# Optimization experiments

Hardware: AMD Instinct MI355X
Metric: run time of the kernel (lower is better)

## Reference

```python
import jax, jax.numpy as jnp
import numpy as np

B, S, H = 2, 1024, 1024
NH, NKV, HD = 16, 4, 64
E, TOPK, I = 8, 2, 3584
EPS = 1e-5
THETA = 1e6


def setup_inputs() -> dict:
    key = jax.random.key(0)
    ks = jax.random.split(key, 12)
    def w(k, shape, fan_in):
        return jax.random.normal(k, shape, dtype=jnp.float32) * (1.0 / np.sqrt(fan_in))
    return {
        "hidden_states": jax.random.normal(ks[0], (B, S, H), dtype=jnp.float32),
        "position_ids": jnp.broadcast_to(jnp.arange(S, dtype=jnp.int64)[None, :], (B, S)),
        "ln1_w": jnp.ones((H,), jnp.float32),
        "ln2_w": jnp.ones((H,), jnp.float32),
        "wq": w(ks[1], (H, NH * HD), H),
        "wk": w(ks[2], (H, NKV * HD), H),
        "wv": w(ks[3], (H, NKV * HD), H),
        "wo": w(ks[4], (NH * HD, H), NH * HD),
        "router_w": w(ks[5], (H, E), H),
        "w_gate": w(ks[6], (E, H, I), H),
        "w_up": w(ks[7], (E, H, I), H),
        "w_down": w(ks[8], (E, I, H), I),
    }


def _rmsnorm(x, w):
    xf = x.astype(jnp.float32)
    return (xf * jax.lax.rsqrt(jnp.mean(xf * xf, -1, keepdims=True) + EPS)).astype(x.dtype) * w


def _rope(x, pos):
    # x: [B,S,nh,HD], pos: [B,S]
    inv_freq = 1.0 / (THETA ** (jnp.arange(0, HD, 2, dtype=jnp.float32) / HD))
    ang = pos.astype(jnp.float32)[..., None] * inv_freq            # [B,S,HD/2]
    emb = jnp.concatenate([ang, ang], axis=-1)                      # [B,S,HD]
    cos, sin = jnp.cos(emb)[:, :, None, :], jnp.sin(emb)[:, :, None, :]
    x1, x2 = x[..., : HD // 2], x[..., HD // 2:]
    rot = jnp.concatenate([-x2, x1], axis=-1)
    return x * cos + rot * sin


def _forward(hidden_states, position_ids, ln1_w, ln2_w, wq, wk, wv, wo,
             router_w, w_gate, w_up, w_down):
    residual = hidden_states
    x = _rmsnorm(hidden_states, ln1_w)

    # ---- attention (GQA, causal, RoPE) ----
    q = (x @ wq).reshape(B, S, NH, HD)
    k = (x @ wk).reshape(B, S, NKV, HD)
    v = (x @ wv).reshape(B, S, NKV, HD)
    q = _rope(q, position_ids)
    k = _rope(k, position_ids)
    rep = NH // NKV
    k = jnp.repeat(k, rep, axis=2)  # [B,S,NH,HD]
    v = jnp.repeat(v, rep, axis=2)
    scores = jnp.einsum("bqhd,bkhd->bhqk", q, k) / np.sqrt(HD)
    causal = jnp.tril(jnp.ones((S, S), bool))
    scores = jnp.where(causal[None, None], scores, jnp.finfo(scores.dtype).min)
    probs = jax.nn.softmax(scores, axis=-1)
    attn = jnp.einsum("bhqk,bkhd->bqhd", probs, v).reshape(B, S, NH * HD)
    hidden = residual + attn @ wo

    # ---- MoE MLP ----
    residual = hidden
    xn = _rmsnorm(hidden, ln2_w).reshape(-1, H)               # [T,H]
    T = xn.shape[0]
    logits = xn @ router_w                                    # [T,E]
    rprobs = jax.nn.softmax(logits.astype(jnp.float32), axis=-1)
    topv, topi = jax.lax.top_k(rprobs, TOPK)                  # [T,TOPK]
    topv = topv / jnp.sum(topv, axis=-1, keepdims=True)       # normalize_top_k_affinities
    weights = jnp.zeros((T, E), jnp.float32).at[jnp.arange(T)[:, None], topi].set(topv)
    g = jnp.einsum("th,ehi->eti", xn, w_gate)                 # [E,T,I]
    u = jnp.einsum("th,ehi->eti", xn, w_up)
    a = jax.nn.silu(g) * u
    eo = jnp.einsum("eti,eih->eth", a, w_down)                # [E,T,H]
    moe = jnp.einsum("eth,te->th", eo, weights).reshape(B, S, H)
    return residual + moe


def reference(hidden_states, position_ids, ln1_w, ln2_w, wq, wk, wv, wo,
              router_w, w_gate, w_up, w_down):
    return _forward(hidden_states, position_ids, ln1_w, ln2_w, wq, wk, wv, wo,
                    router_w, w_gate, w_up, w_down)
```

## Files before the change

kernel.cpp:

```cpp
#include <hip/hip_runtime.h>
#include <hip/hip_bf16.h>
#include <math.h>

#define Bc 2
#define Sc 1024
#define Hc 1024
#define NHc 16
#define NKVc 4
#define HDc 64
#define Ec 8
#define TOPKc 2
#define Ic 3584
#define Tc (Bc*Sc)
#define EPSc 1e-5f

typedef __attribute__((ext_vector_type(8))) short bf16x8;
typedef __attribute__((ext_vector_type(4))) float f32x4;

__device__ __forceinline__ unsigned short f2bf(float f) {
    union { float f; unsigned u; } v; v.f = f;
    unsigned r = v.u + 0x7fffu + ((v.u >> 16) & 1u);
    return (unsigned short)(r >> 16);
}

static const size_t OFF_XN1  = 0;
static const size_t OFF_QB   = 8*1024*1024;
static const size_t OFF_KB   = OFF_QB + 8*1024*1024;
static const size_t OFF_VB   = OFF_KB + 2*1024*1024;
static const size_t OFF_XN2F = OFF_VB + 2*1024*1024;
static const size_t OFF_XN2B = OFF_XN2F + 8*1024*1024;
static const size_t OFF_ACT  = OFF_XN2B + 4*1024*1024;
static const size_t OFF_ROUTE= OFF_ACT + (size_t)4096*3584*2;

__global__ __launch_bounds__(256) void rmsnorm_kernel(const float* __restrict__ x,
        const float* __restrict__ w, float* __restrict__ outf,
        unsigned short* __restrict__ outb) {
    int t = blockIdx.x;
    int tid = threadIdx.x;
    const float* row = x + (size_t)t * Hc;
    float ss = 0.f;
    for (int h = tid; h < Hc; h += 256) { float v = row[h]; ss += v*v; }
    __shared__ float red[256];
    red[tid] = ss; __syncthreads();
    for (int s = 128; s > 0; s >>= 1) { if (tid < s) red[tid] += red[tid+s]; __syncthreads(); }
    float scale = rsqrtf(red[0] / (float)Hc + EPSc);
    for (int h = tid; h < Hc; h += 256) {
        float v = row[h] * scale * w[h];
        outf[(size_t)t*Hc + h] = v;
        if (outb) outb[(size_t)t*Hc + h] = f2bf(v);
    }
}

__global__ __launch_bounds__(256) void qkv_gemm(const float* __restrict__ A,
        const float* __restrict__ wq, const float* __restrict__ wk, const float* __restrict__ wv,
        float* __restrict__ qout, float* __restrict__ kout, float* __restrict__ vout) {
    __shared__ float As[64][17];
    __shared__ float Bs[16][65];
    int n0 = blockIdx.x * 64;
    int m0 = blockIdx.y * 64;
    int tid = threadIdx.x;
    int tx = tid & 15, ty = tid >> 4;
    const float* Bp; int ldb, c0;
    if (n0 < 1024)      { Bp = wq; ldb = 1024; c0 = n0; }
    else if (n0 < 1280) { Bp = wk; ldb = 256;  c0 = n0 - 1024; }
    else                { Bp = wv; ldb = 256;  c0 = n0 - 1280; }
    float acc[4][4] = {};
    for (int k0 = 0; k0 < 1024; k0 += 16) {
        #pragma unroll
        for (int i = 0; i < 4; i++) {
            int lin = tid + i*256; int r = lin >> 4, k = lin & 15;
            As[r][k] = A[(size_t)(m0 + r)*Hc + k0 + k];
        }
        #pragma unroll
        for (int i = 0; i < 4; i++) {
            int lin = tid + i*256; int r = lin >> 6, c = lin & 63;
            Bs[r][c] = Bp[(size_t)(k0 + r)*ldb + c0 + c];
        }
        __syncthreads();
        #pragma unroll
        for (int kk = 0; kk < 16; kk++) {
            float a[4], b[4];
            #pragma unroll
            for (int i = 0; i < 4; i++) a[i] = As[ty*4+i][kk];
            #pragma unroll
            for (int j = 0; j < 4; j++) b[j] = Bs[kk][tx*4+j];
            #pragma unroll
            for (int i = 0; i < 4; i++)
                #pragma unroll
                for (int j = 0; j < 4; j++) acc[i][j] += a[i]*b[j];
        }
        __syncthreads();
    }
    #pragma unroll
    for (int i = 0; i < 4; i++) {
        int m = m0 + ty*4 + i;
        #pragma unroll
        for (int j = 0; j < 4; j++) {
            int n = n0 + tx*4 + j;
            float val = acc[i][j];
            if (n < 1024)      qout[(size_t)m*1024 + n] = val;
            else if (n < 1280) kout[(size_t)m*256 + (n-1024)] = val;
            else               vout[(size_t)m*256 + (n-1280)] = val;
        }
    }
}

__global__ __launch_bounds__(256) void rope_kernel(float* __restrict__ q, float* __restrict__ k) {
    int idx = blockIdx.x*256 + threadIdx.x;
    const int total = Tc*(NHc+NKVc)*32;
    if (idx >= total) return;
    int d = idx & 31;
    int rest = idx >> 5;
    int head = rest % (NHc+NKVc);
    int t = rest / (NHc+NKVc);
    int s = t & (Sc-1);
    float inv = powf(1.0e6f, -(float)d / 32.0f);
    float ang = (float)s * inv;
    float c = cosf(ang), sn = sinf(ang);
    float* base;
    if (head < NHc) base = q + (size_t)t*1024 + head*64;
    else            base = k + (size_t)t*256  + (head-NHc)*64;
    float x1 = base[d], x2 = base[d+32];
    base[d]    = x1*c - x2*sn;
    base[d+32] = x2*c + x1*sn;
}

__global__ __launch_bounds__(256) void attn_kernel(const float* __restrict__ q,
        const float* __restrict__ kbuf, const float* __restrict__ vbuf,
        float* __restrict__ attn) {
    __shared__ float Qs[64][65];
    __shared__ float KVs[64][65];
    __shared__ float Ps[64][65];
    __shared__ float m_s[64], l_s[64], al_s[64];
    int q0 = blockIdx.x * 64;
    int h  = blockIdx.y;
    int b  = blockIdx.z;
    int hk = h >> 2;
    int tid = threadIdx.x;
    int tx = tid & 15, ty = tid >> 4;
    #pragma unroll
    for (int i = 0; i < 16; i++) {
        int lin = tid + i*256; int r = lin >> 6, d = lin & 63;
        Qs[r][d] = q[((size_t)(b*Sc + q0 + r))*1024 + h*64 + d];
    }
    if (tid < 64) { m_s[tid] = -INFINITY; l_s[tid] = 0.f; }
    float O[4][4] = {};
    for (int j0 = 0; j0 <= q0; j0 += 64) {
        __syncthreads();
        #pragma unroll
        for (int i = 0; i < 16; i++) {
            int lin = tid + i*256; int r = lin >> 6, d = lin & 63;
            KVs[r][d] = kbuf[((size_t)(b*Sc + j0 + r))*256 + hk*64 + d];
        }
        __syncthreads();
        float sc[4][4] = {};
        for (int d = 0; d < 64; d++) {
            float a[4], bb[4];
            #pragma unroll
            for (int i = 0; i < 4; i++) a[i] = Qs[ty*4+i][d];
            #pragma unroll
            for (int j = 0; j < 4; j++) bb[j] = KVs[tx*4+j][d];
            #pragma unroll
            for (int i = 0; i < 4; i++)
                #pragma unroll
                for (int j = 0; j < 4; j++) sc[i][j] += a[i]*bb[j];
        }
        bool diag = (j0 == q0);
        #pragma unroll
        for (int i = 0; i < 4; i++) {
            int r = ty*4+i;
            #pragma unroll
            for (int j = 0; j < 4; j++) {
                int c = tx*4+j;
                float v = sc[i][j]*0.125f;
                if (diag && c > r) v = -1e30f;
                Ps[r][c] = v;
            }
        }
        __syncthreads();
        if (tid < 64) {
            int r = tid;
            float mx = -1e30f;
            for (int c = 0; c < 64; c++) mx = fmaxf(mx, Ps[r][c]);
            float newm = fmaxf(m_s[r], mx);
            float alpha = expf(m_s[r] - newm);
            float sum = 0.f;
            for (int c = 0; c < 64; c++) { float p = expf(Ps[r][c] - newm); Ps[r][c] = p; sum += p; }
            l_s[r] = l_s[r]*alpha + sum;
            m_s[r] = newm;
            al_s[r] = alpha;
        }
        #pragma unroll
        for (int i = 0; i < 16; i++) {
            int lin = tid + i*256; int r = lin >> 6, d = lin & 63;
            KVs[r][d] = vbuf[((size_t)(b*Sc + j0 + r))*256 + hk*64 + d];
        }
        __syncthreads();
        #pragma unroll
        for (int i = 0; i < 4; i++) {
            float al = al_s[ty*4+i];
            #pragma unroll
            for (int j = 0; j < 4; j++) O[i][j] *= al;
        }
        for (int c = 0; c < 64; c++) {
            float p[4], vv[4];
            #pragma unroll
            for (int i = 0; i < 4; i++) p[i] = Ps[ty*4+i][c];
            #pragma unroll
            for (int j = 0; j < 4; j++) vv[j] = KVs[c][tx*4+j];
            #pragma unroll
            for (int i = 0; i < 4; i++)
                #pragma unroll
                for (int j = 0; j < 4; j++) O[i][j] += p[i]*vv[j];
        }
    }
    #pragma unroll
    for (int i = 0; i < 4; i++) {
        int r = ty*4+i;
        float inv_l = 1.f / l_s[r];
        int m = b*Sc + q0 + r;
        #pragma unroll
        for (int j = 0; j < 4; j++) {
            int d = tx*4+j;
            attn[(size_t)m*1024 + h*64 + d] = O[i][j]*inv_l;
        }
    }
}

__global__ __launch_bounds__(256) void wo_gemm(const float* __restrict__ A,
        const float* __restrict__ wo, const float* __restrict__ resid,
        float* __restrict__ out) {
    __shared__ float As[64][17];
    __shared__ float Bs[16][65];
    int n0 = blockIdx.x * 64;
    int m0 = blockIdx.y * 64;
    int tid = threadIdx.x;
    int tx = tid & 15, ty = tid >> 4;
    float acc[4][4] = {};
    for (int k0 = 0; k0 < 1024; k0 += 16) {
        #pragma unroll
        for (int i = 0; i < 4; i++) {
            int lin = tid + i*256; int r = lin >> 4, k = lin & 15;
            As[r][k] = A[(size_t)(m0 + r)*Hc + k0 + k];
        }
        #pragma unroll
        for (int i = 0; i < 4; i++) {
            int lin = tid + i*256; int r = lin >> 6, c = lin & 63;
            Bs[r][c] = wo[(size_t)(k0 + r)*Hc + n0 + c];
        }
        __syncthreads();
        #pragma unroll
        for (int kk = 0; kk < 16; kk++) {
            float a[4], b[4];
            #pragma unroll
            for (int i = 0; i < 4; i++) a[i] = As[ty*4+i][kk];
            #pragma unroll
            for (int j = 0; j < 4; j++) b[j] = Bs[kk][tx*4+j];
            #pragma unroll
            for (int i = 0; i < 4; i++)
                #pragma unroll
                for (int j = 0; j < 4; j++) acc[i][j] += a[i]*b[j];
        }
        __syncthreads();
    }
    #pragma unroll
    for (int i = 0; i < 4; i++) {
        int m = m0 + ty*4 + i;
        #pragma unroll
        for (int j = 0; j < 4; j++) {
            int n = n0 + tx*4 + j;
            out[(size_t)m*Hc + n] = acc[i][j] + resid[(size_t)m*Hc + n];
        }
    }
}

__global__ __launch_bounds__(256) void router_kernel(const float* __restrict__ xn2,
        const float* __restrict__ rw, int* __restrict__ counts,
        int* __restrict__ topk_e, float* __restrict__ topk_w) {
    int t = blockIdx.x, tid = threadIdx.x;
    float part[8] = {};
    for (int h = tid; h < 1024; h += 256) {
        float x = xn2[(size_t)t*Hc + h];
        #pragma unroll
        for (int e = 0; e < 8; e++) part[e] += x * rw[h*8 + e];
    }
    __shared__ float red[8][256];
    #pragma unroll
    for (int e = 0; e < 8; e++) red[e][tid] = part[e];
    __syncthreads();
    for (int s = 128; s > 0; s >>= 1) {
        if (tid < s) {
            #pragma unroll
            for (int e = 0; e < 8; e++) red[e][tid] += red[e][tid+s];
        }
        __syncthreads();
    }
    if (tid == 0) {
        float lg[8]; float mx = -1e30f;
        for (int e = 0; e < 8; e++) { lg[e] = red[e][0]; mx = fmaxf(mx, lg[e]); }
        float p[8]; float sum = 0.f;
        for (int e = 0; e < 8; e++) { p[e] = expf(lg[e]-mx); sum += p[e]; }
        for (int e = 0; e < 8; e++) p[e] /= sum;
        int e0 = 0;
        for (int e = 1; e < 8; e++) if (p[e] > p[e0]) e0 = e;
        int e1 = -1;
        for (int e = 0; e < 8; e++) { if (e == e0) continue; if (e1 < 0 || p[e] > p[e1]) e1 = e; }
        float w0 = p[e0], w1 = p[e1]; float wsum = w0 + w1; w0 /= wsum; w1 /= wsum;
        topk_e[t*2] = e0; topk_e[t*2+1] = e1;
        topk_w[t*2] = w0; topk_w[t*2+1] = w1;
        atomicAdd(&counts[e0], 1); atomicAdd(&counts[e1], 1);
    }
}

__global__ void prefix_kernel(const int* __restrict__ counts, int* __restrict__ offsets) {
    if (threadIdx.x == 0 && blockIdx.x == 0) {
        int acc = 0;
        for (int e = 0; e < 8; e++) { offsets[e] = acc; acc += counts[e]; }
    }
}

__global__ __launch_bounds__(256) void fill_kernel(const int* __restrict__ topk_e,
        const float* __restrict__ topk_w, const int* __restrict__ offsets,
        int* __restrict__ fill, int* __restrict__ list_tok, float* __restrict__ list_w) {
    int t = blockIdx.x*256 + threadIdx.x;
    if (t >= Tc) return;
    #pragma unroll
    for (int j = 0; j < 2; j++) {
        int e = topk_e[t*2+j]; float w = topk_w[t*2+j];
        int slot = atomicAdd(&fill[e], 1);
        list_tok[offsets[e]+slot] = t;
        list_w[offsets[e]+slot] = w;
    }
}

__global__ __launch_bounds__(256) void gemm_gateup(const unsigned short* __restrict__ xn2b,
        const float* __restrict__ wg, const float* __restrict__ wu,
        const int* __restrict__ counts, const int* __restrict__ offsets,
        const int* __restrict__ list_tok, unsigned short* __restrict__ act) {
    int e = blockIdx.z;
    int cnt = counts[e];
    int m0 = blockIdx.y * 64;
    if (m0 >= cnt) return;
    int n0 = blockIdx.x * 128;
    int aoff = offsets[e];
    __shared__ unsigned short As[64*40];
    __shared__ unsigned short Bg[128*40];
    __shared__ unsigned short Bu[128*40];
    __shared__ int toks[64];
    int tid = threadIdx.x;
    if (tid < 64) toks[tid] = list_tok[aoff + min(m0 + tid, cnt-1)];
    __syncthreads();
    const float* Bgp = wg + (size_t)e*Hc*Ic + n0;
    const float* Bup = wu + (size_t)e*Hc*Ic + n0;
    int lane = tid & 63, wave = tid >> 6;
    int wm = wave >> 1, wn = wave & 1;
    int ml = lane & 15, quad = lane >> 4;
    f32x4 accg[2][4] = {}, accu[2][4] = {};
    for (int k0 = 0; k0 < Hc; k0 += 32) {
        {
            int r = tid >> 2, part = tid & 3;
            uint4 v = *reinterpret_cast<const uint4*>(xn2b + (size_t)toks[r]*Hc + k0 + part*8);
            *reinterpret_cast<uint4*>(&As[r*40 + part*8]) = v;
        }
        #pragma unroll
        for (int it = 0; it < 8; it++) {
            int lin = tid + it*256;
            int n = lin & 127, kp = lin >> 7;
            float g0 = Bgp[(size_t)(k0 + 2*kp)*Ic + n];
            float g1 = Bgp[(size_t)(k0 + 2*kp + 1)*Ic + n];
            float u0 = Bup[(size_t)(k0 + 2*kp)*Ic + n];
            float u1 = Bup[(size_t)(k0 + 2*kp + 1)*Ic + n];
            *reinterpret_cast<unsigned*>(&Bg[n*40 + 2*kp]) = (unsigned)f2bf(g0) | ((unsigned)f2bf(g1) << 16);
            *reinterpret_cast<unsigned*>(&Bu[n*40 + 2*kp]) = (unsigned)f2bf(u0) | ((unsigned)f2bf(u1) << 16);
        }
        __syncthreads();
        bf16x8 a[2], bg[4], bu[4];
        #pragma unroll
        for (int mt = 0; mt < 2; mt++)
            a[mt] = *reinterpret_cast<const bf16x8*>(&As[(wm*32 + mt*16 + ml)*40 + quad*8]);
        #pragma unroll
        for (int nt = 0; nt < 4; nt++) {
            bg[nt] = *reinterpret_cast<const bf16x8*>(&Bg[(wn*64 + nt*16 + ml)*40 + quad*8]);
            bu[nt] = *reinterpret_cast<const bf16x8*>(&Bu[(wn*64 + nt*16 + ml)*40 + quad*8]);
        }
        #pragma unroll
        for (int mt = 0; mt < 2; mt++)
            #pragma unroll
            for (int nt = 0; nt < 4; nt++) {
                accg[mt][nt] = __builtin_amdgcn_mfma_f32_16x16x32_bf16(a[mt], bg[nt], accg[mt][nt], 0, 0, 0);
                accu[mt][nt] = __builtin_amdgcn_mfma_f32_16x16x32_bf16(a[mt], bu[nt], accu[mt][nt], 0, 0, 0);
            }
        __syncthreads();
    }
    #pragma unroll
    for (int mt = 0; mt < 2; mt++)
        #pragma unroll
        for (int nt = 0; nt < 4; nt++)
            #pragma unroll
            for (int rg = 0; rg < 4; rg++) {
                int rowl = wm*32 + mt*16 + quad*4 + rg;
                if (m0 + rowl < cnt) {
                    int n = n0 + wn*64 + nt*16 + ml;
                    float g = accg[mt][nt][rg], u = accu[mt][nt][rg];
                    float sg = g / (1.f + expf(-g));
                    act[(size_t)(aoff + m0 + rowl)*Ic + n] = f2bf(sg * u);
                }
            }
}

__global__ __launch_bounds__(256) void gemm_down(const unsigned short* __restrict__ act,
        const float* __restrict__ wd, const int* __restrict__ counts,
        const int* __restrict__ offsets, const int* __restrict__ list_tok,
        const float* __restrict__ list_w, float* __restrict__ out) {
    int e = blockIdx.z;
    int cnt = counts[e];
    int m0 = blockIdx.y * 128;
    if (m0 >= cnt) return;
    int n0 = blockIdx.x * 128;
    int aoff = offsets[e];
    __shared__ unsigned short As[128*40];
    __shared__ unsigned short Bs[128*40];
    const unsigned short* A = act + (size_t)(aoff + m0)*Ic;
    const float* B = wd + (size_t)e*Ic*Hc + n0;
    int rowclamp = cnt - 1 - m0;
    int tid = threadIdx.x;
    int lane = tid & 63, wave = tid >> 6;
    int wm = wave >> 1, wn = wave & 1;
    int ml = lane & 15, quad = lane >> 4;
    f32x4 acc[4][4] = {};
    for (int k0 = 0; k0 < Ic; k0 += 32) {
        #pragma unroll
        for (int it = 0; it < 2; it++) {
            int lin = tid + it*256;
            int r = lin >> 2, part = lin & 3;
            int rc = min(r, rowclamp);
            uint4 v = *reinterpret_cast<const uint4*>(A + (size_t)rc*Ic + k0 + part*8);
            *reinterpret_cast<uint4*>(&As[r*40 + part*8]) = v;
        }
        #pragma unroll
        for (int it = 0; it < 8; it++) {
            int lin = tid + it*256;
            int n = lin & 127, kp = lin >> 7;
            float b0 = B[(size_t)(k0 + 2*kp)*Hc + n];
            float b1 = B[(size_t)(k0 + 2*kp + 1)*Hc + n];
            *reinterpret_cast<unsigned*>(&Bs[n*40 + 2*kp]) = (unsigned)f2bf(b0) | ((unsigned)f2bf(b1) << 16);
        }
        __syncthreads();
        bf16x8 a[4], b[4];
        #pragma unroll
        for (int mt = 0; mt < 4; mt++)
            a[mt] = *reinterpret_cast<const bf16x8*>(&As[(wm*64 + mt*16 + ml)*40 + quad*8]);
        #pragma unroll
        for (int nt = 0; nt < 4; nt++)
            b[nt] = *reinterpret_cast<const bf16x8*>(&Bs[(wn*64 + nt*16 + ml)*40 + quad*8]);
        #pragma unroll
        for (int mt = 0; mt < 4; mt++)
            #pragma unroll
            for (int nt = 0; nt < 4; nt++)
                acc[mt][nt] = __builtin_amdgcn_mfma_f32_16x16x32_bf16(a[mt], b[nt], acc[mt][nt], 0, 0, 0);
        __syncthreads();
    }
    #pragma unroll
    for (int mt = 0; mt < 4; mt++)
        #pragma unroll
        for (int nt = 0; nt < 4; nt++)
            #pragma unroll
            for (int rg = 0; rg < 4; rg++) {
                int rowl = wm*64 + mt*16 + quad*4 + rg;
                if (m0 + rowl < cnt) {
                    int t = list_tok[aoff + m0 + rowl];
                    float w = list_w[aoff + m0 + rowl];
                    int n = n0 + wn*64 + nt*16 + ml;
                    atomicAdd(&out[(size_t)t*Hc + n], w * acc[mt][nt][rg]);
                }
            }
}

extern "C" void kernel_launch(void* const* d_in, const int* in_sizes, int n_in,
                              void* d_out, int out_size, void* d_ws, size_t ws_size,
                              hipStream_t stream) {
    const float* hidden = (const float*)d_in[0];
    const float* ln1 = (const float*)d_in[2];
    const float* ln2 = (const float*)d_in[3];
    const float* wq  = (const float*)d_in[4];
    const float* wk  = (const float*)d_in[5];
    const float* wv  = (const float*)d_in[6];
    const float* wo  = (const float*)d_in[7];
    const float* rw  = (const float*)d_in[8];
    const float* wg  = (const float*)d_in[9];
    const float* wu  = (const float*)d_in[10];
    const float* wd  = (const float*)d_in[11];
    float* out = (float*)d_out;
    char* ws = (char*)d_ws;

    float* xn1f  = (float*)(ws + OFF_XN1);
    float* attnf = xn1f;
    float* qb    = (float*)(ws + OFF_QB);
    float* kb    = (float*)(ws + OFF_KB);
    float* vb    = (float*)(ws + OFF_VB);
    float* xn2f  = (float*)(ws + OFF_XN2F);
    unsigned short* xn2b = (unsigned short*)(ws + OFF_XN2B);
    unsigned short* act  = (unsigned short*)(ws + OFF_ACT);
    int*   route    = (int*)(ws + OFF_ROUTE);
    int*   counts   = route;
    int*   fillc    = route + 8;
    int*   offsets  = route + 16;
    int*   topk_e   = route + 24;
    float* topk_w   = (float*)(route + 24 + 2*Tc);
    int*   list_tok = route + 24 + 4*Tc;
    float* list_w   = (float*)(route + 24 + 6*Tc);

    hipMemsetAsync(counts, 0, 16*sizeof(int), stream);

    rmsnorm_kernel<<<Tc, 256, 0, stream>>>(hidden, ln1, xn1f, nullptr);
    qkv_gemm<<<dim3(24, 32), 256, 0, stream>>>(xn1f, wq, wk, wv, qb, kb, vb);
    rope_kernel<<<(Tc*(NHc+NKVc)*32 + 255)/256, 256, 0, stream>>>(qb, kb);
    attn_kernel<<<dim3(16, 16, 2), 256, 0, stream>>>(qb, kb, vb, attnf);
    wo_gemm<<<dim3(16, 32), 256, 0, stream>>>(attnf, wo, hidden, out);
    rmsnorm_kernel<<<Tc, 256, 0, stream>>>(out, ln2, xn2f, xn2b);
    router_kernel<<<Tc, 256, 0, stream>>>(xn2f, rw, counts, topk_e, topk_w);
    prefix_kernel<<<1, 64, 0, stream>>>(counts, offsets);
    fill_kernel<<<(Tc+255)/256, 256, 0, stream>>>(topk_e, topk_w, offsets, fillc, list_tok, list_w);
    gemm_gateup<<<dim3(28, 64, 8), 256, 0, stream>>>(xn2b, wg, wu, counts, offsets, list_tok, act);
    gemm_down<<<dim3(8, 32, 8), 256, 0, stream>>>(act, wd, counts, offsets, list_tok, list_w, out);
}
```

Before: 1.248 ms.

## Vectorize fp32 weight loads with packed bf16 convert and retile MoE gate/up GEMM

The gate/up and down GEMMs now load fp32 weights as 16-byte vectors along N and convert them with the hardware packed bf16 instruction, replacing scalar loads and software rounding. The gate/up tile changes from 64x128 to 128x64 so more tokens share each weight fetch. The intent is to cut the cost of streaming the large expert weights. The y grids shrink to match the per-expert token counts, and RoPE's powf is replaced with exp2f. The LDS stores become more scattered, and the hardware convert's rounding may differ slightly from the old software rounding.

Result: no change. 1.244 ms (-0.3%).

```diff
diff --git a/kernel.cpp b/kernel.cpp
--- a/kernel.cpp
+++ b/kernel.cpp
@@ -21,6 +21,12 @@
     union { float f; unsigned u; } v; v.f = f;
     unsigned r = v.u + 0x7fffu + ((v.u >> 16) & 1u);
     return (unsigned short)(r >> 16);
+}
+
+__device__ __forceinline__ unsigned cvt_pk_bf16(float lo, float hi) {
+    unsigned r;
+    asm("v_cvt_pk_bf16_f32 %0, %1, %2" : "=v"(r) : "v"(lo), "v"(hi));
+    return r;
 }
 
 static const size_t OFF_XN1  = 0;
@@ -114,7 +120,7 @@
     int head = rest % (NHc+NKVc);
     int t = rest / (NHc+NKVc);
     int s = t & (Sc-1);
-    float inv = powf(1.0e6f, -(float)d / 32.0f);
+    float inv = exp2f(-(float)d * 0.62286152f);
     float ang = (float)s * inv;
     float c = cosf(ang), sn = sinf(ang);
     float* base;
@@ -339,68 +345,73 @@
         const int* __restrict__ list_tok, unsigned short* __restrict__ act) {
     int e = blockIdx.z;
     int cnt = counts[e];
-    int m0 = blockIdx.y * 64;
+    int m0 = blockIdx.y * 128;
     if (m0 >= cnt) return;
-    int n0 = blockIdx.x * 128;
+    int n0 = blockIdx.x * 64;
     int aoff = offsets[e];
-    __shared__ unsigned short As[64*40];
-    __shared__ unsigned short Bg[128*40];
-    __shared__ unsigned short Bu[128*40];
-    __shared__ int toks[64];
+    __shared__ unsigned short As[128*40];
+    __shared__ unsigned short Bg[64*40];
+    __shared__ unsigned short Bu[64*40];
+    __shared__ int toks[128];
     int tid = threadIdx.x;
-    if (tid < 64) toks[tid] = list_tok[aoff + min(m0 + tid, cnt-1)];
+    if (tid < 128) toks[tid] = list_tok[aoff + min(m0 + tid, cnt-1)];
     __syncthreads();
     const float* Bgp = wg + (size_t)e*Hc*Ic + n0;
     const float* Bup = wu + (size_t)e*Hc*Ic + n0;
     int lane = tid & 63, wave = tid >> 6;
     int wm = wave >> 1, wn = wave & 1;
     int ml = lane & 15, quad = lane >> 4;
-    f32x4 accg[2][4] = {}, accu[2][4] = {};
+    int kp = tid & 15, n4 = tid >> 4;
+    f32x4 accg[4][2] = {}, accu[4][2] = {};
     for (int k0 = 0; k0 < Hc; k0 += 32) {
-        {
-            int r = tid >> 2, part = tid & 3;
+        #pragma unroll
+        for (int it = 0; it < 2; it++) {
+            int lin = tid + it*256;
+            int r = lin >> 2, part = lin & 3;
             uint4 v = *reinterpret_cast<const uint4*>(xn2b + (size_t)toks[r]*Hc + k0 + part*8);
             *reinterpret_cast<uint4*>(&As[r*40 + part*8]) = v;
         }
-        #pragma unroll
-        for (int it = 0; it < 8; it++) {
-            int lin = tid + it*256;
-            int n = lin & 127, kp = lin >> 7;
-            float g0 = Bgp[(size_t)(k0 + 2*kp)*Ic + n];
-            float g1 = Bgp[(size_t)(k0 + 2*kp + 1)*Ic + n];
-            float u0 = Bup[(size_t)(k0 + 2*kp)*Ic + n];
-            float u1 = Bup[(size_t)(k0 + 2*kp + 1)*Ic + n];
-            *reinterpret_cast<unsigned*>(&Bg[n*40 + 2*kp]) = (unsigned)f2bf(g0) | ((unsigned)f2bf(g1) << 16);
-            *reinterpret_cast<unsigned*>(&Bu[n*40 + 2*kp]) = (unsigned)f2bf(u0) | ((unsigned)f2bf(u1) << 16);
-        }
-        __syncthreads();
-        bf16x8 a[2], bg[4], bu[4];
-        #pragma unroll
-        for (int mt = 0; mt < 2; mt++)
-            a[mt] = *reinterpret_cast<const bf16x8*>(&As[(wm*32 + mt*16 + ml)*40 + quad*8]);
-        #pragma unroll
-        for (int nt = 0; nt < 4; nt++) {
-            bg[nt] = *reinterpret_cast<const bf16x8*>(&Bg[(wn*64 + nt*16 + ml)*40 + quad*8]);
-            bu[nt] = *reinterpret_cast<const bf16x8*>(&Bu[(wn*64 + nt*16 + ml)*40 + quad*8]);
-        }
-        #pragma unroll
-        for (int mt = 0; mt < 2; mt++)
-            #pragma unroll
-            for (int nt = 0; nt < 4; nt++) {
+        {
+            const float* gp = Bgp + (size_t)(k0 + 2*kp)*Ic + n4*4;
+            const float* up = Bup + (size_t)(k0 + 2*kp)*Ic + n4*4;
+            f32x4 g0 = *reinterpret_cast<const f32x4*>(gp);
+            f32x4 g1 = *reinterpret_cast<const f32x4*>(gp + Ic);
+            f32x4 u0 = *reinterpret_cast<const f32x4*>(up);
+            f32x4 u1 = *reinterpret_cast<const f32x4*>(up + Ic);
+            #pragma unroll
+            for (int j = 0; j < 4; j++) {
+                *reinterpret_cast<unsigned*>(&Bg[(n4*4+j)*40 + 2*kp]) = cvt_pk_bf16(g0[j], g1[j]);
+                *reinterpret_cast<unsigned*>(&Bu[(n4*4+j)*40 + 2*kp]) = cvt_pk_bf16(u0[j], u1[j]);
+            }
+        }
+        __syncthreads();
+        bf16x8 a[4], bg[2], bu[2];
+        #pragma unroll
+        for (int mt = 0; mt < 4; mt++)
+            a[mt] = *reinterpret_cast<const bf16x8*>(&As[(wm*64 + mt*16 + ml)*40 + quad*8]);
+        #pragma unroll
+        for (int nt = 0; nt < 2; nt++) {
+            bg[nt] = *reinterpret_cast<const bf16x8*>(&Bg[(wn*32 + nt*16 + ml)*40 + quad*8]);
+            bu[nt] = *reinterpret_cast<const bf16x8*>(&Bu[(wn*32 + nt*16 + ml)*40 + quad*8]);
+        }
+        #pragma unroll
+        for (int mt = 0; mt < 4; mt++)
+            #pragma unroll
+            for (int nt = 0; nt < 2; nt++) {
                 accg[mt][nt] = __builtin_amdgcn_mfma_f32_16x16x32_bf16(a[mt], bg[nt], accg[mt][nt], 0, 0, 0);
                 accu[mt][nt] = __builtin_amdgcn_mfma_f32_16x16x32_bf16(a[mt], bu[nt], accu[mt][nt], 0, 0, 0);
             }
         __syncthreads();
     }
     #pragma unroll
-    for (int mt = 0; mt < 2; mt++)
-        #pragma unroll
-        for (int nt = 0; nt < 4; nt++)
+    for (int mt = 0; mt < 4; mt++)
+        #pragma unroll
+        for (int nt = 0; nt < 2; nt++)
             #pragma unroll
             for (int rg = 0; rg < 4; rg++) {
-                int rowl = wm*32 + mt*16 + quad*4 + rg;
+                int rowl = wm*64 + mt*16 + quad*4 + rg;
                 if (m0 + rowl < cnt) {
-                    int n = n0 + wn*64 + nt*16 + ml;
+                    int n = n0 + wn*32 + nt*16 + ml;
                     float g = accg[mt][nt][rg], u = accu[mt][nt][rg];
                     float sg = g / (1.f + expf(-g));
                     act[(size_t)(aoff + m0 + rowl)*Ic + n] = f2bf(sg * u);
@@ -438,12 +449,15 @@
             *reinterpret_cast<uint4*>(&As[r*40 + part*8]) = v;
         }
         #pragma unroll
-        for (int it = 0; it < 8; it++) {
+        for (int it = 0; it < 2; it++) {
             int lin = tid + it*256;
-            int n = lin & 127, kp = lin >> 7;
-            float b0 = B[(size_t)(k0 + 2*kp)*Hc + n];
-            float b1 = B[(size_t)(k0 + 2*kp + 1)*Hc + n];
-            *reinterpret_cast<unsigned*>(&Bs[n*40 + 2*kp]) = (unsigned)f2bf(b0) | ((unsigned)f2bf(b1) << 16);
+            int kp = lin & 15, n4 = lin >> 4;
+            const float* bp = B + (size_t)(k0 + 2*kp)*Hc + n4*4;
+            f32x4 b0 = *reinterpret_cast<const f32x4*>(bp);
+            f32x4 b1 = *reinterpret_cast<const f32x4*>(bp + Hc);
+            #pragma unroll
+            for (int j = 0; j < 4; j++)
+                *reinterpret_cast<unsigned*>(&Bs[(n4*4+j)*40 + 2*kp]) = cvt_pk_bf16(b0[j], b1[j]);
         }
         __syncthreads();
         bf16x8 a[4], b[4];
@@ -521,6 +535,6 @@
     router_kernel<<<Tc, 256, 0, stream>>>(xn2f, rw, counts, topk_e, topk_w);
     prefix_kernel<<<1, 64, 0, stream>>>(counts, offsets);
     fill_kernel<<<(Tc+255)/256, 256, 0, stream>>>(topk_e, topk_w, offsets, fillc, list_tok, list_w);
-    gemm_gateup<<<dim3(28, 64, 8), 256, 0, stream>>>(xn2b, wg, wu, counts, offsets, list_tok, act);
-    gemm_down<<<dim3(8, 32, 8), 256, 0, stream>>>(act, wd, counts, offsets, list_tok, list_w, out);
-}
+    gemm_gateup<<<dim3(56, 16, 8), 256, 0, stream>>>(xn2b, wg, wu, counts, offsets, list_tok, act);
+    gemm_down<<<dim3(8, 16, 8), 256, 0, stream>>>(act, wd, counts, offsets, list_tok, list_w, out);
+}
```
